# Optimization experiments

Hardware: AMD Instinct MI355X
Metric: run time of the kernel (lower is better)

Reference implementation:

```python
import jax, jax.numpy as jnp
import numpy as np

N_NODES = 10000
DIM_IN = 64
DIM_OUT = 64
K = 3
BATCH = 32
N_EDGES = 160000


def setup_inputs() -> dict:
    key = jax.random.key(0)
    ks = jax.random.split(key, 8)
    inputs = jax.random.normal(ks[0], (BATCH, N_NODES, DIM_IN), dtype=jnp.float32)
    hx = jax.random.normal(ks[1], (BATCH, N_NODES, DIM_OUT), dtype=jnp.float32)
    edge_index = jax.random.randint(ks[2], (2, N_EDGES), 0, N_NODES, dtype=jnp.int64)
    edge_weight = jax.random.uniform(ks[3], (N_EDGES,), dtype=jnp.float32)
    f = K * (DIM_IN + DIM_OUT)
    # xavier-uniform style scaling
    lim_g = float(np.sqrt(6.0 / (2 * DIM_OUT + f)))
    lim_c = float(np.sqrt(6.0 / (DIM_OUT + f)))
    weight_gate = jax.random.uniform(ks[4], (2 * DIM_OUT, f), minval=-lim_g, maxval=lim_g, dtype=jnp.float32)
    weight_candidate = jax.random.uniform(ks[5], (DIM_OUT, f), minval=-lim_c, maxval=lim_c, dtype=jnp.float32)
    bias_gate = jnp.zeros((2 * DIM_OUT,), dtype=jnp.float32)
    bias_candidate = jnp.zeros((DIM_OUT,), dtype=jnp.float32)
    return {
        'inputs': inputs, 'hx': hx, 'edge_index': edge_index, 'edge_weight': edge_weight,
        'weight_gate': weight_gate, 'weight_candidate': weight_candidate,
        'bias_gate': bias_gate, 'bias_candidate': bias_candidate,
    }


def _graph_conv(x, row, col, w):
    # x: [B, N, F]; out[b, dst] += w_e * x[b, src]; src=col, dst=row
    gathered = x[:, col, :] * w[None, :, None]  # [B, E, F]
    return jnp.zeros_like(x).at[:, row, :].add(gathered)


def _diffusion_conv(x, row, col, w, K):
    results = [x]
    x0 = x
    x1 = _graph_conv(x0, row, col, w)
    results.append(x1)
    for k in range(2, K):
        xk = 2.0 * _graph_conv(x1, row, col, w) - x0
        results.append(xk)
        x0, x1 = x1, xk
    return jnp.concatenate(results, axis=-1)  # [B, N, K*F]


def reference(inputs, hx, edge_index, edge_weight, weight_gate, weight_candidate, bias_gate, bias_candidate):
    row, col = edge_index[0], edge_index[1]
    hidden_dim = hx.shape[-1]
    x = jnp.concatenate([inputs, hx], axis=-1)
    x_diff = _diffusion_conv(x, row, col, edge_weight, K)
    gates = jnp.einsum('bnf,gf->bng', x_diff, weight_gate) + bias_gate
    z_r = jax.nn.sigmoid(gates)
    z, r = z_r[..., :hidden_dim], z_r[..., hidden_dim:]
    x_cand = jnp.concatenate([inputs, r * hx], axis=-1)
    x_cand_diff = _diffusion_conv(x_cand, row, col, edge_weight, K)
    cand = jnp.tanh(jnp.einsum('bnf,of->bno', x_cand_diff, weight_candidate) + bias_candidate)
    return (1.0 - z) * hx + z * cand
```

## Files before the change

### kernel.cpp

```cpp
#include <hip/hip_runtime.h>
#include <math.h>
#include <stdint.h>

#define NN   10000
#define EE   160000
#define BB   32
#define FDIM 384
#define EE_PAD (EE + 4 * NN)
#define NB_FULL 1250
#define NB_HALF 625

typedef _Float16 f16x8 __attribute__((ext_vector_type(8)));
typedef _Float16 f16x4 __attribute__((ext_vector_type(4)));
typedef _Float16 f16x2 __attribute__((ext_vector_type(2)));
typedef __fp16   pk16  __attribute__((ext_vector_type(2)));
typedef float    f32x4 __attribute__((ext_vector_type(4)));


__global__ void count_kernel(const int* __restrict__ ei, int* __restrict__ counts) {
    int e = blockIdx.x * blockDim.x + threadIdx.x;
    if (e < EE) atomicAdd(&counts[ei[e]], 1);
}

__global__ void scan_kernel(const int* __restrict__ counts, int* __restrict__ row_ptr) {
    __shared__ int sh[1024];
    int t = threadIdx.x;
    const int CH = 10;
    int base = t * CH;
    int local[CH];
    int s = 0;
#pragma unroll
    for (int i = 0; i < CH; i++) {
        int idx = base + i;
        int v = (idx < NN) ? ((counts[idx] + 3) & ~3) : 0;
        local[i] = v; s += v;
    }
    sh[t] = s;
    __syncthreads();
    for (int off = 1; off < 1024; off <<= 1) {
        int add = (t >= off) ? sh[t - off] : 0;
        __syncthreads();
        sh[t] += add;
        __syncthreads();
    }
    int prefix = (t == 0) ? 0 : sh[t - 1];
#pragma unroll
    for (int i = 0; i < CH; i++) {
        int idx = base + i;
        if (idx < NN) row_ptr[idx] = prefix;
        prefix += local[i];
    }
    if (t == 1023) row_ptr[NN] = prefix;
}

__global__ void fill_kernel(const int* __restrict__ ei, const float* __restrict__ ew,
                            const int* __restrict__ row_ptr, int* __restrict__ cursor,
                            int* __restrict__ col_s, _Float16* __restrict__ w_h) {
    int e = blockIdx.x * blockDim.x + threadIdx.x;
    if (e < EE) {
        int r = ei[e];
        int c = ei[EE + e];
        int pos = row_ptr[r] + atomicAdd(&cursor[r], 1);
        col_s[pos] = c;
        w_h[pos] = (_Float16)ew[e];
    }
}


__global__ void wconv_kernel(const float* __restrict__ wg, const float* __restrict__ wc,
                             _Float16* __restrict__ whg, _Float16* __restrict__ whc) {
    int i = blockIdx.x * blockDim.x + threadIdx.x;
    if (i < 128 * FDIM) whg[i] = (_Float16)wg[i];
    if (i < 64 * FDIM)  whc[i] = (_Float16)wc[i];
}

__global__ void cvt_h_kernel(const float* __restrict__ a, const float* __restrict__ b,
                             _Float16* __restrict__ ah, _Float16* __restrict__ bh, int n4) {
    int i = blockIdx.x * blockDim.x + threadIdx.x;
    if (i >= n4) return;
    const float* s = (blockIdx.y == 0) ? a : b;
    _Float16*    d = (blockIdx.y == 0) ? ah : bh;
    float4 v = reinterpret_cast<const float4*>(s)[i];
    f16x4 h; h[0] = (_Float16)v.x; h[1] = (_Float16)v.y;
             h[2] = (_Float16)v.z; h[3] = (_Float16)v.w;
    reinterpret_cast<f16x4*>(d)[i] = h;
}

__device__ inline void sp_map(int NB, int bc_n, int& b, int& nb) {
    int L = blockIdx.x;
    if ((bc_n & 7) == 0) {
        int xcd = L & 7;
        int x   = L >> 3;
        b  = xcd + 8 * (x / NB);
        nb = x % NB;
    } else {
        b  = L / NB;
        nb = L % NB;
    }
}

__device__ __forceinline__ void gather_acc4(
        const int* __restrict__ col_s, const _Float16* __restrict__ w_h,
        const char* __restrict__ srcb, int sh, unsigned fo_all,
        int start, int end, float& a0, float& a1, float& a2, float& a3)
{
#if __has_builtin(__builtin_amdgcn_fdot2) && __has_builtin(__builtin_amdgcn_perm)
#define GDOT(da, db, wp)                                                              \
    a0 = __builtin_amdgcn_fdot2(__builtin_bit_cast(pk16,                              \
             __builtin_amdgcn_perm(db.x, da.x, 0x05040100u)), wp, a0, false);         \
    a1 = __builtin_amdgcn_fdot2(__builtin_bit_cast(pk16,                              \
             __builtin_amdgcn_perm(db.x, da.x, 0x07060302u)), wp, a1, false);         \
    a2 = __builtin_amdgcn_fdot2(__builtin_bit_cast(pk16,                              \
             __builtin_amdgcn_perm(db.y, da.y, 0x05040100u)), wp, a2, false);         \
    a3 = __builtin_amdgcn_fdot2(__builtin_bit_cast(pk16,                              \
             __builtin_amdgcn_perm(db.y, da.y, 0x07060302u)), wp, a3, false);
#define GLD(c) *reinterpret_cast<const uint2*>(srcb + (((unsigned)(c) << sh) + fo_all))
    int j = start;
    for (; j + 16 <= end; j += 16) {
        int4  ca = *reinterpret_cast<const int4*>(&col_s[j]);
        int4  cb = *reinterpret_cast<const int4*>(&col_s[j + 4]);
        int4  cc = *reinterpret_cast<const int4*>(&col_s[j + 8]);
        int4  cd = *reinterpret_cast<const int4*>(&col_s[j + 12]);
        uint2 wv0 = *reinterpret_cast<const uint2*>(&w_h[j]);
        uint2 wv1 = *reinterpret_cast<const uint2*>(&w_h[j + 4]);
        uint2 wv2 = *reinterpret_cast<const uint2*>(&w_h[j + 8]);
        uint2 wv3 = *reinterpret_cast<const uint2*>(&w_h[j + 12]);
        uint2 d0 = GLD(ca.x), d1 = GLD(ca.y), d2 = GLD(ca.z), d3 = GLD(ca.w);
        uint2 d4 = GLD(cb.x), d5 = GLD(cb.y), d6 = GLD(cb.z), d7 = GLD(cb.w);
        uint2 d8 = GLD(cc.x), d9 = GLD(cc.y), da_ = GLD(cc.z), db_ = GLD(cc.w);
        uint2 dc_ = GLD(cd.x), dd_ = GLD(cd.y), de_ = GLD(cd.z), df_ = GLD(cd.w);
        GDOT(d0, d1, __builtin_bit_cast(pk16, wv0.x))
        GDOT(d2, d3, __builtin_bit_cast(pk16, wv0.y))
        GDOT(d4, d5, __builtin_bit_cast(pk16, wv1.x))
        GDOT(d6, d7, __builtin_bit_cast(pk16, wv1.y))
        GDOT(d8, d9, __builtin_bit_cast(pk16, wv2.x))
        GDOT(da_, db_, __builtin_bit_cast(pk16, wv2.y))
        GDOT(dc_, dd_, __builtin_bit_cast(pk16, wv3.x))
        GDOT(de_, df_, __builtin_bit_cast(pk16, wv3.y))
    }
    if (j + 8 <= end) {
        int4  ca = *reinterpret_cast<const int4*>(&col_s[j]);
        int4  cb = *reinterpret_cast<const int4*>(&col_s[j + 4]);
        uint2 wv0 = *reinterpret_cast<const uint2*>(&w_h[j]);
        uint2 wv1 = *reinterpret_cast<const uint2*>(&w_h[j + 4]);
        uint2 d0 = GLD(ca.x), d1 = GLD(ca.y), d2 = GLD(ca.z), d3 = GLD(ca.w);
        uint2 d4 = GLD(cb.x), d5 = GLD(cb.y), d6 = GLD(cb.z), d7 = GLD(cb.w);
        GDOT(d0, d1, __builtin_bit_cast(pk16, wv0.x))
        GDOT(d2, d3, __builtin_bit_cast(pk16, wv0.y))
        GDOT(d4, d5, __builtin_bit_cast(pk16, wv1.x))
        GDOT(d6, d7, __builtin_bit_cast(pk16, wv1.y))
        j += 8;
    }
    if (j < end) {
        int4  ca = *reinterpret_cast<const int4*>(&col_s[j]);
        uint2 wv0 = *reinterpret_cast<const uint2*>(&w_h[j]);
        uint2 d0 = GLD(ca.x), d1 = GLD(ca.y), d2 = GLD(ca.z), d3 = GLD(ca.w);
        GDOT(d0, d1, __builtin_bit_cast(pk16, wv0.x))
        GDOT(d2, d3, __builtin_bit_cast(pk16, wv0.y))
    }
#undef GLD
#undef GDOT
#else
    for (int j = start; j < end; ++j) {
        int c = col_s[j]; float w = (float)w_h[j];
        f16x4 v = *reinterpret_cast<const f16x4*>(srcb + (((unsigned)c << sh) + fo_all));
        a0 += w * (float)v[0]; a1 += w * (float)v[1];
        a2 += w * (float)v[2]; a3 += w * (float)v[3];
    }
#endif
}

__global__ __launch_bounds__(256)
void spmm_full16(const int* __restrict__ row_ptr, const int* __restrict__ col_s,
                 const _Float16* __restrict__ w_h,
                 const _Float16* __restrict__ srcBase, int sh, int deltaB,
                 const _Float16* __restrict__ subA, const _Float16* __restrict__ subB,
                 float alpha, _Float16* __restrict__ outbuf, int bc_n) {
    int b, nb; sp_map(NB_FULL, bc_n, b, nb);
    int node = nb * 8 + (threadIdx.x >> 5);
    int g    = threadIdx.x & 31;
    int fo, db;
    if (g < 16) { fo = g * 4;        db = 0;      }
    else        { fo = (g - 16) * 4; db = deltaB; }
    unsigned fo_all = ((unsigned)(b * NN) << sh) + (unsigned)db + (unsigned)(fo * 2);
    int start = row_ptr[node], end = row_ptr[node + 1];
    long base = (long)b * NN;
    float a0 = 0.f, a1 = 0.f, a2 = 0.f, a3 = 0.f;
    gather_acc4(col_s, w_h, (const char*)srcBase, sh, fo_all, start, end, a0, a1, a2, a3);
    a0 *= alpha; a1 *= alpha; a2 *= alpha; a3 *= alpha;
    if (subA) {
        const _Float16* sub = (g < 16) ? subA : subB;
        f16x4 s = *reinterpret_cast<const f16x4*>(&sub[(base + node) * 64 + fo]);
        a0 -= (float)s[0]; a1 -= (float)s[1]; a2 -= (float)s[2]; a3 -= (float)s[3];
    }
    f16x4 r; r[0] = (_Float16)a0; r[1] = (_Float16)a1;
             r[2] = (_Float16)a2; r[3] = (_Float16)a3;
    *reinterpret_cast<f16x4*>(&outbuf[(base + node) * 128 + g * 4]) = r;
}

__global__ __launch_bounds__(256)
void spmm_half16(const int* __restrict__ row_ptr, const int* __restrict__ col_s,
                 const _Float16* __restrict__ w_h,
                 const _Float16* __restrict__ src, int sh,
                 const _Float16* __restrict__ sub, float alpha,
                 _Float16* __restrict__ outbuf, int bc_n) {
    int b, nb; sp_map(NB_HALF, bc_n, b, nb);
    int node = nb * 16 + (threadIdx.x >> 4);
    int fo   = (threadIdx.x & 15) * 4;
    unsigned fo_all = ((unsigned)(b * NN) << sh) + (unsigned)(fo * 2);
    int start = row_ptr[node], end = row_ptr[node + 1];
    long base = (long)b * NN;
    float a0 = 0.f, a1 = 0.f, a2 = 0.f, a3 = 0.f;
    gather_acc4(col_s, w_h, (const char*)src, sh, fo_all, start, end, a0, a1, a2, a3);
    a0 *= alpha; a1 *= alpha; a2 *= alpha; a3 *= alpha;
    if (sub) {
        f16x4 s = *reinterpret_cast<const f16x4*>(&sub[(base + node) * 64 + fo]);
        a0 -= (float)s[0]; a1 -= (float)s[1]; a2 -= (float)s[2]; a3 -= (float)s[3];
    }
    f16x4 r; r[0] = (_Float16)a0; r[1] = (_Float16)a1;
             r[2] = (_Float16)a2; r[3] = (_Float16)a3;
    *reinterpret_cast<f16x4*>(&outbuf[(base + node) * 128 + fo]) = r;
}

template <int MODE>
__global__ __launch_bounds__(256)
void gemm_mfma(const _Float16* __restrict__ in_h,
               const _Float16* __restrict__ hxl_h,
               const _Float16* __restrict__ W1h,
               const _Float16* __restrict__ W2h,
               const _Float16* __restrict__ Wh,
               const float* __restrict__ bias,
               const float* __restrict__ hx32,
               const _Float16* __restrict__ zbuf,
               float* __restrict__ outf,
               _Float16* __restrict__ z_o,
               _Float16* __restrict__ rh_o,
               int Mchunk)
{
    const int NOUT = (MODE == 0) ? 128 : 64;
    const int TNF  = NOUT / 16;
    const int PIT  = 40;

    __shared__ _Float16 Alds[64 * PIT];
    __shared__ _Float16 Blds[NOUT * PIT];

    int tid  = threadIdx.x;
    int lane = tid & 63;
    int w    = tid >> 6;
    int lr   = lane & 15;
    int lko  = (lane >> 4) * 8;

    long mbase = (long)blockIdx.x * 64;

    f32x4 acc[TNF];
#pragma unroll
    for (int f = 0; f < TNF; f++) acc[f] = (f32x4){0.f, 0.f, 0.f, 0.f};

    for (int k0 = 0; k0 < FDIM; k0 += 32) {
        const _Float16* src; int stride; int koff;
        if      (k0 < 64)  { src = in_h;  stride = 64;  koff = 0;   }
        else if (k0 < 128) { src = hxl_h; stride = 64;  koff = 64;  }
        else if (k0 < 256) { src = W1h;   stride = 128; koff = 128; }
        else               { src = W2h;   stride = 128; koff = 256; }

        {
            int rr = tid >> 2;
            int q  = tid & 3;
            long row = mbase + rr;
            if (row >= Mchunk) row = Mchunk - 1;
            *reinterpret_cast<f16x8*>(&Alds[rr * PIT + q * 8]) =
                *reinterpret_cast<const f16x8*>(&src[row * (long)stride + (k0 - koff) + q * 8]);
        }
        {
            for (int l = tid * 8; l < NOUT * 32; l += 256 * 8) {
                int n  = l >> 5;
                int kk = l & 31;
                *reinterpret_cast<f16x8*>(&Blds[n * PIT + kk]) =
                    *reinterpret_cast<const f16x8*>(&Wh[n * FDIM + k0 + kk]);
            }
        }
        __syncthreads();

        f16x8 a = *reinterpret_cast<const f16x8*>(&Alds[(w * 16 + lr) * PIT + lko]);
#pragma unroll
        for (int f = 0; f < TNF; f++) {
            f16x8 bfr = *reinterpret_cast<const f16x8*>(&Blds[(lr + 16 * f) * PIT + lko]);
            acc[f] = __builtin_amdgcn_mfma_f32_16x16x32_f16(a, bfr, acc[f], 0, 0, 0);
        }
        __syncthreads();
    }

#pragma unroll
    for (int f = 0; f < TNF; f++) {
        int g = lr + 16 * f;
#pragma unroll
        for (int j = 0; j < 4; j++) {
            long m = mbase + w * 16 + (lane >> 4) * 4 + j;
            if (m >= Mchunk) continue;
            float v = acc[f][j] + bias[g];
            if (MODE == 0) {
                float s = 1.f / (1.f + __expf(-v));
                if (g < 64) z_o[m * 64 + g] = (_Float16)s;
                else        rh_o[m * 64 + (g - 64)] = (_Float16)(s * hx32[m * 64 + (g - 64)]);
            } else {
                float cnd = tanhf(v);
                float zz = (float)zbuf[m * 64 + g];
                outf[m * 64 + g] = (1.f - zz) * hx32[m * 64 + g] + zz * cnd;
            }
        }
    }
}


extern "C" void kernel_launch(void* const* d_in, const int* in_sizes, int n_in,
                              void* d_out, int out_size, void* d_ws, size_t ws_size,
                              hipStream_t stream) {
    const float* inputs = (const float*)d_in[0];
    const float* hx     = (const float*)d_in[1];
    const int*   ei     = (const int*)d_in[2];
    const float* ew     = (const float*)d_in[3];
    const float* wg     = (const float*)d_in[4];
    const float* wc     = (const float*)d_in[5];
    const float* bg     = (const float*)d_in[6];
    const float* bc     = (const float*)d_in[7];
    float* out = (float*)d_out;

    const size_t csr_bytes = (size_t)(NN + 1) * 4 + (size_t)NN * 4 * 2
                           + (size_t)EE_PAD * 6
                           + (size_t)(128 + 64) * FDIM * 2 + 512;
    const size_t per_batch = (size_t)NN * 512 * 2;

    int bc_n = 1;
    const int cand[6] = {32, 16, 8, 4, 2, 1};
    for (int i = 0; i < 6; i++) {
        if (csr_bytes + (size_t)cand[i] * per_batch <= ws_size) { bc_n = cand[i]; break; }
    }

    uint8_t* p = (uint8_t*)d_ws;
    _Float16* W1h  = (_Float16*)p; p += (size_t)bc_n * NN * 128 * 2;
    _Float16* W2h  = (_Float16*)p; p += (size_t)bc_n * NN * 128 * 2;
    _Float16* in_h = (_Float16*)p; p += (size_t)bc_n * NN * 64 * 2;
    _Float16* hx_h = (_Float16*)p; p += (size_t)bc_n * NN * 64 * 2;
    _Float16* rh   = (_Float16*)p; p += (size_t)bc_n * NN * 64 * 2;
    _Float16* zh   = (_Float16*)p; p += (size_t)bc_n * NN * 64 * 2;
    int* row_ptr = (int*)p;  p += (size_t)(NN + 1) * 4;
    p = (uint8_t*)(((uintptr_t)p + 15) & ~(uintptr_t)15);
    int* counts  = (int*)p;  p += (size_t)NN * 4;
    int* cursor  = (int*)p;  p += (size_t)NN * 4;
    int* col_s   = (int*)p;  p += (size_t)EE_PAD * 4;
    _Float16* w_h = (_Float16*)p; p += (size_t)EE_PAD * 2;
    p = (uint8_t*)(((uintptr_t)p + 63) & ~(uintptr_t)63);
    _Float16* whg = (_Float16*)p; p += (size_t)128 * FDIM * 2;
    _Float16* whc = (_Float16*)p;

    hipMemsetAsync(counts, 0, (size_t)NN * 8 + (size_t)EE_PAD * 6, stream);
    count_kernel<<<(EE + 255) / 256, 256, 0, stream>>>(ei, counts);
    scan_kernel<<<1, 1024, 0, stream>>>(counts, row_ptr);
    fill_kernel<<<(EE + 255) / 256, 256, 0, stream>>>(ei, ew, row_ptr, cursor, col_s, w_h);
    wconv_kernel<<<(128 * FDIM + 255) / 256, 256, 0, stream>>>(wg, wc, whg, whc);

    for (int b0 = 0; b0 < BB; b0 += bc_n) {
        const float* in_c = inputs + (size_t)b0 * NN * 64;
        const float* hx_c = hx     + (size_t)b0 * NN * 64;
        float*       out_c = out   + (size_t)b0 * NN * 64;
        int Mchunk = bc_n * NN;
        int gemm_blocks = (Mchunk + 63) / 64;
        int n4 = bc_n * NN * 64 / 4;

        dim3 cg((n4 + 255) / 256, 2);
        cvt_h_kernel<<<cg, 256, 0, stream>>>(in_c, hx_c, in_h, hx_h, n4);

        int deltaA = (int)((const char*)hx_h - (const char*)in_h);

        spmm_full16<<<NB_FULL * bc_n, 256, 0, stream>>>(row_ptr, col_s, w_h,
                                                        in_h, 7, deltaA,
                                                        nullptr, nullptr, 1.f, W1h, bc_n);
        spmm_full16<<<NB_FULL * bc_n, 256, 0, stream>>>(row_ptr, col_s, w_h,
                                                        W1h, 8, 128,
                                                        in_h, hx_h, 2.f, W2h, bc_n);
        gemm_mfma<0><<<gemm_blocks, 256, 0, stream>>>(in_h, hx_h, W1h, W2h, whg, bg,
                                                      hx_c, nullptr, nullptr, zh, rh, Mchunk);
        spmm_half16<<<NB_HALF * bc_n, 256, 0, stream>>>(row_ptr, col_s, w_h, rh, 7,
                                                        nullptr, 1.f, W1h + 64, bc_n);
        spmm_half16<<<NB_HALF * bc_n, 256, 0, stream>>>(row_ptr, col_s, w_h, W1h + 64, 8,
                                                        rh, 2.f, W2h + 64, bc_n);
        gemm_mfma<1><<<gemm_blocks, 256, 0, stream>>>(in_h, rh, W1h, W2h, whc, bc,
                                                      hx_c, zh, out_c, nullptr, nullptr, Mchunk);
    }
}
```

Before: 960.7 us.

## Enlarge GEMM tile to 128 rows with 512 threads; shrink SpMM gather unroll

The MFMA GEMM now uses 128-row tiles with 512 threads per block, so each weight (B) tile load into LDS is shared by twice as many rows, and the grid is halved. The SpMM gather loop drops its 16-edge unroll and iterates in 8-edge steps, which lowers register pressure at the cost of less memory-level parallelism per thread. The A-tile load index (tid>>2) now covers 128 rows, and the B load becomes a single guarded iteration since 512*8 covers NOUT*32.

Result: faster. 910.7 us (-5.2%).

```diff
diff --git a/kernel.cpp b/kernel.cpp
--- a/kernel.cpp
+++ b/kernel.cpp
@@ -116,29 +116,7 @@
              __builtin_amdgcn_perm(db.y, da.y, 0x07060302u)), wp, a3, false);
 #define GLD(c) *reinterpret_cast<const uint2*>(srcb + (((unsigned)(c) << sh) + fo_all))
     int j = start;
-    for (; j + 16 <= end; j += 16) {
-        int4  ca = *reinterpret_cast<const int4*>(&col_s[j]);
-        int4  cb = *reinterpret_cast<const int4*>(&col_s[j + 4]);
-        int4  cc = *reinterpret_cast<const int4*>(&col_s[j + 8]);
-        int4  cd = *reinterpret_cast<const int4*>(&col_s[j + 12]);
-        uint2 wv0 = *reinterpret_cast<const uint2*>(&w_h[j]);
-        uint2 wv1 = *reinterpret_cast<const uint2*>(&w_h[j + 4]);
-        uint2 wv2 = *reinterpret_cast<const uint2*>(&w_h[j + 8]);
-        uint2 wv3 = *reinterpret_cast<const uint2*>(&w_h[j + 12]);
-        uint2 d0 = GLD(ca.x), d1 = GLD(ca.y), d2 = GLD(ca.z), d3 = GLD(ca.w);
-        uint2 d4 = GLD(cb.x), d5 = GLD(cb.y), d6 = GLD(cb.z), d7 = GLD(cb.w);
-        uint2 d8 = GLD(cc.x), d9 = GLD(cc.y), da_ = GLD(cc.z), db_ = GLD(cc.w);
-        uint2 dc_ = GLD(cd.x), dd_ = GLD(cd.y), de_ = GLD(cd.z), df_ = GLD(cd.w);
-        GDOT(d0, d1, __builtin_bit_cast(pk16, wv0.x))
-        GDOT(d2, d3, __builtin_bit_cast(pk16, wv0.y))
-        GDOT(d4, d5, __builtin_bit_cast(pk16, wv1.x))
-        GDOT(d6, d7, __builtin_bit_cast(pk16, wv1.y))
-        GDOT(d8, d9, __builtin_bit_cast(pk16, wv2.x))
-        GDOT(da_, db_, __builtin_bit_cast(pk16, wv2.y))
-        GDOT(dc_, dd_, __builtin_bit_cast(pk16, wv3.x))
-        GDOT(de_, df_, __builtin_bit_cast(pk16, wv3.y))
-    }
-    if (j + 8 <= end) {
+    for (; j + 8 <= end; j += 8) {
         int4  ca = *reinterpret_cast<const int4*>(&col_s[j]);
         int4  cb = *reinterpret_cast<const int4*>(&col_s[j + 4]);
         uint2 wv0 = *reinterpret_cast<const uint2*>(&w_h[j]);
@@ -149,7 +127,6 @@
         GDOT(d2, d3, __builtin_bit_cast(pk16, wv0.y))
         GDOT(d4, d5, __builtin_bit_cast(pk16, wv1.x))
         GDOT(d6, d7, __builtin_bit_cast(pk16, wv1.y))
-        j += 8;
     }
     if (j < end) {
         int4  ca = *reinterpret_cast<const int4*>(&col_s[j]);
@@ -223,7 +200,7 @@
 }
 
 template <int MODE>
-__global__ __launch_bounds__(256)
+__global__ __launch_bounds__(512)
 void gemm_mfma(const _Float16* __restrict__ in_h,
                const _Float16* __restrict__ hxl_h,
                const _Float16* __restrict__ W1h,
@@ -240,8 +217,9 @@
     const int NOUT = (MODE == 0) ? 128 : 64;
     const int TNF  = NOUT / 16;
     const int PIT  = 40;
-
-    __shared__ _Float16 Alds[64 * PIT];
+    const int BM   = 128;
+
+    __shared__ _Float16 Alds[BM * PIT];
     __shared__ _Float16 Blds[NOUT * PIT];
 
     int tid  = threadIdx.x;
@@ -250,7 +228,7 @@
     int lr   = lane & 15;
     int lko  = (lane >> 4) * 8;
 
-    long mbase = (long)blockIdx.x * 64;
+    long mbase = (long)blockIdx.x * BM;
 
     f32x4 acc[TNF];
 #pragma unroll
@@ -272,7 +250,8 @@
                 *reinterpret_cast<const f16x8*>(&src[row * (long)stride + (k0 - koff) + q * 8]);
         }
         {
-            for (int l = tid * 8; l < NOUT * 32; l += 256 * 8) {
+            int l = tid * 8;
+            if (l < NOUT * 32) {
                 int n  = l >> 5;
                 int kk = l & 31;
                 *reinterpret_cast<f16x8*>(&Blds[n * PIT + kk]) =
@@ -364,7 +343,7 @@
         const float* hx_c = hx     + (size_t)b0 * NN * 64;
         float*       out_c = out   + (size_t)b0 * NN * 64;
         int Mchunk = bc_n * NN;
-        int gemm_blocks = (Mchunk + 63) / 64;
+        int gemm_blocks = (Mchunk + 127) / 128;
         int n4 = bc_n * NN * 64 / 4;
 
         dim3 cg((n4 + 255) / 256, 2);
@@ -378,13 +357,13 @@
         spmm_full16<<<NB_FULL * bc_n, 256, 0, stream>>>(row_ptr, col_s, w_h,
                                                         W1h, 8, 128,
                                                         in_h, hx_h, 2.f, W2h, bc_n);
-        gemm_mfma<0><<<gemm_blocks, 256, 0, stream>>>(in_h, hx_h, W1h, W2h, whg, bg,
+        gemm_mfma<0><<<gemm_blocks, 512, 0, stream>>>(in_h, hx_h, W1h, W2h, whg, bg,
                                                       hx_c, nullptr, nullptr, zh, rh, Mchunk);
         spmm_half16<<<NB_HALF * bc_n, 256, 0, stream>>>(row_ptr, col_s, w_h, rh, 7,
                                                         nullptr, 1.f, W1h + 64, bc_n);
         spmm_half16<<<NB_HALF * bc_n, 256, 0, stream>>>(row_ptr, col_s, w_h, W1h + 64, 8,
                                                         rh, 2.f, W2h + 64, bc_n);
-        gemm_mfma<1><<<gemm_blocks, 256, 0, stream>>>(in_h, rh, W1h, W2h, whc, bc,
+        gemm_mfma<1><<<gemm_blocks, 512, 0, stream>>>(in_h, rh, W1h, W2h, whc, bc,
                                                       hx_c, zh, out_c, nullptr, nullptr, Mchunk);
     }
 }
```
